# Performance work log

Measured on AMD Instinct MI355X. Metric: run time of the kernel, lower is better.

The kernel has to match this reference:

```python
import jax, jax.numpy as jnp
import numpy as np

B, NPG, A, E = 128, 512, 8, 504   # graphs, nodes/graph, agents, edges/graph
F_IN, HID, H = 3, 64, 8
C = HID
F = H * C                          # 512 = concat head output
OUT = 2
NEG_SLOPE = 0.2


def _seg_softmax(alpha, dst, n):
    # edge-softmax normalized over destination-node neighborhoods
    m = jax.ops.segment_max(alpha, dst, num_segments=n)
    e = jnp.exp(alpha - m[dst])
    s = jax.ops.segment_sum(e, dst, num_segments=n)
    return e / jnp.clip(s[dst], 1e-16)


def _gat(x, src, dst, ea, W, b, a_s, a_d, We, a_e, n, self_loops):
    # PyG GATConv: heads=H, concat=True, edge_dim=1, fill_value='mean'
    xs = (x @ W).reshape(n, H, C)                      # [N,H,C]
    als = jnp.einsum('nhc,hc->nh', xs, a_s)            # alpha_src per node
    ald = jnp.einsum('nhc,hc->nh', xs, a_d)            # alpha_dst per node
    if self_loops:
        # fill_value='mean': self-loop attr = mean of incoming edge attrs
        ssum = jax.ops.segment_sum(ea, dst, num_segments=n)
        cnt = jax.ops.segment_sum(jnp.ones((dst.shape[0], 1), ea.dtype), dst, num_segments=n)
        loop_attr = ssum / jnp.maximum(cnt, 1.0)
        ea = jnp.concatenate([ea, loop_attr], axis=0)
        loop = jnp.arange(n, dtype=src.dtype)
        src = jnp.concatenate([src, loop])
        dst = jnp.concatenate([dst, loop])
    ee = (ea @ We).reshape(-1, H, C)                   # lin_edge
    ale = jnp.einsum('ehc,hc->eh', ee, a_e)            # alpha_edge per edge
    alpha = jax.nn.leaky_relu(als[src] + ald[dst] + ale, NEG_SLOPE)  # [E,H]
    alpha = _seg_softmax(alpha, dst, n)
    out = jax.ops.segment_sum(alpha[:, :, None] * xs[src], dst, num_segments=n)
    return out.reshape(n, H * C) + b


def _forward(x, edge_index, edge_attr, p1, p2, p3, fc1_w, fc1_b, fc2_w, fc2_b):
    Bq, npg, _ = x.shape
    n = Bq * npg
    off = (jnp.arange(Bq, dtype=edge_index.dtype) * npg)[:, None]   # PyG Batch offsets
    src = (edge_index[..., 0] + off).reshape(-1)
    dst = (edge_index[..., 1] + off).reshape(-1)
    ea = edge_attr.reshape(-1, 1)
    h = x.reshape(n, -1)
    h = jax.nn.relu(_gat(h, src, dst, ea, *p1, n, False))   # conv1: add_self_loops=False
    h = jax.nn.relu(_gat(h, src, dst, ea, *p2, n, True))
    h = jax.nn.relu(_gat(h, src, dst, ea, *p3, n, True))
    hg = h.reshape(Bq, npg, F)
    graph_emb = hg.mean(axis=1)                      # global_mean_pool (equal-size graphs)
    agent_emb = hg[:, :A].reshape(Bq * A, F)         # first num_agents nodes per graph
    comb = jnp.concatenate([agent_emb, jnp.repeat(graph_emb, A, axis=0)], axis=1)
    comb = jax.nn.relu(comb @ fc1_w + fc1_b)         # fc1 ReLU (extra torch.relu is idempotent)
    pred = comb @ fc2_w + fc2_b
    return pred.reshape(Bq, A, OUT)


def setup_inputs() -> dict:
    key = jax.random.key(0)
    ks = jax.random.split(key, 32)
    rn = lambda i, shape: jax.random.normal(ks[i], shape, jnp.float32) * 0.05
    inp = {
        'x': jax.random.normal(ks[0], (B, NPG, F_IN), jnp.float32),
        'edge_index': jax.random.randint(ks[1], (B, E, 2), 0, NPG, jnp.int32),
        'edge_attr': jax.random.normal(ks[2], (B, E, 1), jnp.float32),
    }
    dims = [F_IN, F, F]
    for li, din in enumerate(dims, start=1):
        inp[f'W{li}'] = rn(3 + li * 6, (din, H * C))
        inp[f'b{li}'] = jnp.zeros((H * C,), jnp.float32)
        inp[f'as{li}'] = rn(4 + li * 6, (H, C))
        inp[f'ad{li}'] = rn(5 + li * 6, (H, C))
        inp[f'We{li}'] = rn(6 + li * 6, (1, H * C))
        inp[f'ae{li}'] = rn(7 + li * 6, (H, C))
    inp['fc1_w'] = rn(28, (2 * F, 4 * HID))
    inp['fc1_b'] = jnp.zeros((4 * HID,), jnp.float32)
    inp['fc2_w'] = rn(29, (4 * HID, OUT))
    inp['fc2_b'] = jnp.zeros((OUT,), jnp.float32)
    return inp


def reference(x, edge_index, edge_attr,
              W1, b1, as1, ad1, We1, ae1,
              W2, b2, as2, ad2, We2, ae2,
              W3, b3, as3, ad3, We3, ae3,
              fc1_w, fc1_b, fc2_w, fc2_b):
    p1 = (W1, b1, as1, ad1, We1, ae1)
    p2 = (W2, b2, as2, ad2, We2, ae2)
    p3 = (W3, b3, as3, ad3, We3, ae3)
    return _forward(x, edge_index, edge_attr, p1, p2, p3, fc1_w, fc1_b, fc2_w, fc2_b)
```

## Files before the change

kernel.cpp:

```cpp
#include <hip/hip_runtime.h>
#include <hip/hip_bf16.h>
#include <math.h>

#define NGRAPH 128
#define NPG_   512
#define NN     (NGRAPH*NPG_)
#define EPG    504
#define ETOT   (NGRAPH*EPG)
#define HEADS  8
#define FDIM   512
#define NEG    0.2f

typedef __hip_bfloat16 bf16;
typedef __attribute__((ext_vector_type(8))) short short8;
typedef __attribute__((ext_vector_type(4))) float f32x4;

static __device__ __forceinline__ float bf(short s){
  union { unsigned u; float f; } c; c.u = ((unsigned)(unsigned short)s) << 16; return c.f;
}
static __device__ __forceinline__ short fbf(float v){
  bf16 b = __float2bfloat16(v); return *(short*)&b;
}

static __device__ __forceinline__ void gload16(void* lds, const void* g){
  __builtin_amdgcn_global_load_lds((const __attribute__((address_space(1))) void*)g,
                                   (__attribute__((address_space(3))) void*)lds, 16, 0, 0);
}

__global__ void k_sentinel(float* out, int n){
  int i = blockIdx.x*blockDim.x + threadIdx.x;
  if (i < n) out[i] = 12345.0f;
}

__global__ __launch_bounds__(512) void k_csr(const int* __restrict__ ei, const float* __restrict__ ea,
                                             const float* __restrict__ We0, const float* __restrict__ ae0,
                                             const float* __restrict__ We1, const float* __restrict__ ae1,
                                             const float* __restrict__ We2, const float* __restrict__ ae2,
                                             int* __restrict__ deg_g, int* __restrict__ row_ptr,
                                             float* __restrict__ la,
                                             int* __restrict__ esrc, float* __restrict__ eattr,
                                             float* __restrict__ coef){
  int b = blockIdx.x;
  int t = threadIdx.x;
  if (b >= NGRAPH){
    int l = b - NGRAPH;
    const float* We = l==0 ? We0 : (l==1 ? We1 : We2);
    const float* ae = l==0 ? ae0 : (l==1 ? ae1 : ae2);
    float v = We[t]*ae[t];
    #pragma unroll
    for (int o=32;o>0;o>>=1) v += __shfl_down(v, o);
    if ((t & 63) == 0) coef[l*HEADS + (t>>6)] = v;
    return;
  }
  __shared__ int   dg[512];
  __shared__ float ss[512];
  __shared__ int   scan[512];
  __shared__ int   cur[512];
  dg[t] = 0; ss[t] = 0.f;
  __syncthreads();
  int src=0, dst=0; float at=0.f;
  if (t < EPG){
    src = ei[(b*EPG+t)*2];
    dst = ei[(b*EPG+t)*2+1];
    at  = ea[b*EPG+t];
    atomicAdd(&dg[dst], 1);
    atomicAdd(&ss[dst], at);
  }
  __syncthreads();
  int d = dg[t];
  scan[t] = d;
  __syncthreads();
  for (int o=1;o<512;o<<=1){
    int v2 = (t>=o) ? scan[t-o] : 0;
    __syncthreads();
    scan[t] += v2;
    __syncthreads();
  }
  int excl = scan[t] - d;
  int n = b*NPG_ + t;
  row_ptr[n] = b*EPG + excl;
  deg_g[n]   = d;
  la[n]      = ss[t] / fmaxf((float)d, 1.f);
  cur[t] = excl;
  __syncthreads();
  if (t < EPG){
    int slot = atomicAdd(&cur[dst], 1);
    int p = b*EPG + slot;
    esrc[p]  = b*NPG_ + src;
    eattr[p] = at;
  }
}

__global__ void k_wt(const float* __restrict__ W1, const float* __restrict__ W2,
                     bf16* __restrict__ wt){
  int idx = blockIdx.x*blockDim.x + threadIdx.x;
  if (idx >= 2*FDIM*FDIM) return;
  int l = idx >> 18;
  int r = idx & (FDIM*FDIM-1);
  int n = r >> 9, k = r & 511;
  const float* W = l ? W2 : W1;
  wt[idx] = __float2bfloat16(W[k*FDIM + n]);
}

__global__ __launch_bounds__(256) void k_gat1(const float* __restrict__ x,
                                              const float* __restrict__ W,
                                              const float* __restrict__ a_s,
                                              const float* __restrict__ a_d,
                                              const float* __restrict__ coef,
                                              const int* __restrict__ row_ptr,
                                              const int* __restrict__ deg,
                                              const int* __restrict__ esrc,
                                              const float* __restrict__ eattr,
                                              const float* __restrict__ bias,
                                              bf16* __restrict__ h){
  int nwg = gridDim.x;
  int cpx = nwg >> 3;
  int bid = blockIdx.x;
  int swz = (bid & 7)*cpx + (bid >> 3);
  int n = swz*4 + (threadIdx.x >> 6);
  int lane = threadIdx.x & 63;
  int hh = lane >> 3;
  int f0 = lane << 3;

  float w0[8], w1[8], w2[8], as8[8], ad8[8];
  #pragma unroll
  for (int j=0;j<8;j+=4){
    *(float4*)&w0[j]  = *(const float4*)&W[f0+j];
    *(float4*)&w1[j]  = *(const float4*)&W[FDIM+f0+j];
    *(float4*)&w2[j]  = *(const float4*)&W[2*FDIM+f0+j];
    *(float4*)&as8[j] = *(const float4*)&a_s[f0+j];
    *(float4*)&ad8[j] = *(const float4*)&a_d[f0+j];
  }

  const float* xr = x + n*3;
  float x0 = xr[0], x1 = xr[1], x2 = xr[2];
  float dsum = 0.f;
  #pragma unroll
  for (int j=0;j<8;j++){
    float v = x0*w0[j] + x1*w1[j] + x2*w2[j];
    dsum += v*ad8[j];
  }
  #pragma unroll
  for (int o=1;o<8;o<<=1) dsum += __shfl_xor(dsum, o);
  float aldn = dsum;
  float ch = coef[hh];

  int row = row_ptr[n], d = deg[n];
  float m = -1e30f, ssum = 0.f;
  float acc[8] = {};
  for (int i=0;i<d;i++){
    int s = esrc[row+i]; float at = eattr[row+i];
    const float* xsr = x + s*3;
    float y0 = xsr[0], y1 = xsr[1], y2 = xsr[2];
    float v[8]; float ssrc = 0.f;
    #pragma unroll
    for (int j=0;j<8;j++){
      v[j] = y0*w0[j] + y1*w1[j] + y2*w2[j];
      ssrc += v[j]*as8[j];
    }
    #pragma unroll
    for (int o=1;o<8;o<<=1) ssrc += __shfl_xor(ssrc, o);
    float raw = ssrc + aldn + at*ch;
    raw = raw > 0.f ? raw : NEG*raw;
    float mn = fmaxf(m, raw);
    float sc = __expf(m - mn);
    float p  = __expf(raw - mn);
    ssum = ssum*sc + p;
    #pragma unroll
    for (int j=0;j<8;j++) acc[j] = acc[j]*sc + p*v[j];
    m = mn;
  }
  float inv = 1.f / fmaxf(ssum, 1e-16f);
  short8 r;
  #pragma unroll
  for (int j=0;j<8;j++){
    float o = acc[j]*inv + bias[f0+j];
    r[j] = fbf(o > 0.f ? o : 0.f);
  }
  ((short8*)(h + (size_t)n*FDIM))[lane] = r;
}

__global__ __launch_bounds__(256) void k_attn_node(const bf16* __restrict__ xs,
                                                   const float* __restrict__ a_s,
                                                   const float* __restrict__ a_d,
                                                   float* __restrict__ als,
                                                   float* __restrict__ ald){
  int n = blockIdx.x*4 + (threadIdx.x >> 6);
  int lane = threadIdx.x & 63;
  short8 v = ((const short8*)(xs + (size_t)n*FDIM))[lane];
  const float4* as4 = (const float4*)a_s;
  const float4* ad4 = (const float4*)a_d;
  float4 sa = as4[lane*2], sb = as4[lane*2+1];
  float4 da = ad4[lane*2], db = ad4[lane*2+1];
  float s = bf(v[0])*sa.x + bf(v[1])*sa.y + bf(v[2])*sa.z + bf(v[3])*sa.w
          + bf(v[4])*sb.x + bf(v[5])*sb.y + bf(v[6])*sb.z + bf(v[7])*sb.w;
  float d = bf(v[0])*da.x + bf(v[1])*da.y + bf(v[2])*da.z + bf(v[3])*da.w
          + bf(v[4])*db.x + bf(v[5])*db.y + bf(v[6])*db.z + bf(v[7])*db.w;
  #pragma unroll
  for (int o=1;o<8;o<<=1){ s += __shfl_xor(s, o); d += __shfl_xor(d, o); }
  if ((lane & 7) == 0){
    int hh = lane >> 3;
    als[n*HEADS+hh] = s;
    ald[n*HEADS+hh] = d;
  }
}

__global__ __launch_bounds__(256) void k_gat(const bf16* __restrict__ xs,
                                             const float* __restrict__ als,
                                             const float* __restrict__ ald,
                                             const float* __restrict__ coef,
                                             const int* __restrict__ row_ptr,
                                             const int* __restrict__ deg,
                                             const int* __restrict__ esrc,
                                             const float* __restrict__ eattr,
                                             const float* __restrict__ la,
                                             const float* __restrict__ bias,
                                             bf16* __restrict__ h){
  int nwg = gridDim.x;
  int cpx = nwg >> 3;
  int bid = blockIdx.x;
  int swz = (bid & 7)*cpx + (bid >> 3);
  int n = swz*4 + (threadIdx.x >> 6);
  int lane = threadIdx.x & 63;
  int hh = lane >> 3;
  int row = row_ptr[n], d = deg[n];
  int tot = d + 1;
  float aldn = ald[n*HEADS+hh];
  float ch = coef[hh];
  float lan = la[n];

  float m = -1e30f, ssum = 0.f;
  float acc[8] = {};
  for (int i=0;i<tot;i++){
    int s; float at;
    if (i<d){ s = esrc[row+i]; at = eattr[row+i]; }
    else    { s = n;           at = lan; }
    float raw = als[s*HEADS+hh] + aldn + at*ch;
    raw = raw > 0.f ? raw : NEG*raw;
    float mn = fmaxf(m, raw);
    float scale = __expf(m - mn);
    float p = __expf(raw - mn);
    ssum = ssum*scale + p;
    short8 v = ((const short8*)(xs + (size_t)s*FDIM))[lane];
    #pragma unroll
    for (int j=0;j<8;j++) acc[j] = acc[j]*scale + p*bf(v[j]);
    m = mn;
  }
  float inv = 1.f / fmaxf(ssum, 1e-16f);
  const float4* b4 = (const float4*)bias;
  float4 ba = b4[lane*2], bb = b4[lane*2+1];
  float bias8[8] = {ba.x,ba.y,ba.z,ba.w,bb.x,bb.y,bb.z,bb.w};
  short8 r;
  #pragma unroll
  for (int j=0;j<8;j++){
    float o = acc[j]*inv + bias8[j];
    r[j] = fbf(o > 0.f ? o : 0.f);
  }
  ((short8*)(h + (size_t)n*FDIM))[lane] = r;
}

__global__ __launch_bounds__(256) void gemm_mfma(const bf16* __restrict__ A,
                                                 const bf16* __restrict__ Wt,
                                                 bf16* __restrict__ C,
                                                 int M, int N, int K){
  __shared__ short As[128*64];
  __shared__ short Bs[128*64];
  int bid = blockIdx.x;
  int wk = ((bid & 7) << 8) | (bid >> 3);
  const int bm = (wk >> 2)*128, bn = (wk & 3)*128;
  const int tid = threadIdx.x;
  const int lane = tid & 63;
  const int w = tid >> 6;
  const int wm = (w >> 1)*64, wn = (w & 1)*64;
  const int lr = lane & 15;
  const int lk = lane >> 4;

  f32x4 acc[4][4] = {};

  for (int k0 = 0; k0 < K; k0 += 64){
    #pragma unroll
    for (int is = 0; is < 4; ++is){
      int i = is*256 + tid;
      int r = i >> 3, g = i & 7;
      int gs = g ^ (r & 7);
      gload16(&As[i*8], A  + (size_t)(bm+r)*K + k0 + gs*8);
      gload16(&Bs[i*8], Wt + (size_t)(bn+r)*K + k0 + gs*8);
    }
    __syncthreads();
    #pragma unroll
    for (int kk = 0; kk < 2; ++kk){
      short8 af[4], bfr[4];
      #pragma unroll
      for (int mi=0; mi<4; ++mi){
        int row = wm + mi*16 + lr;
        int g = (kk*4 + lk) ^ (row & 7);
        af[mi] = *(const short8*)&As[row*64 + g*8];
      }
      #pragma unroll
      for (int ni=0; ni<4; ++ni){
        int row = wn + ni*16 + lr;
        int g = (kk*4 + lk) ^ (row & 7);
        bfr[ni] = *(const short8*)&Bs[row*64 + g*8];
      }
      #pragma unroll
      for (int mi=0; mi<4; ++mi)
        #pragma unroll
        for (int ni=0; ni<4; ++ni)
          acc[mi][ni] = __builtin_amdgcn_mfma_f32_16x16x32_bf16(af[mi], bfr[ni], acc[mi][ni], 0,0,0);
    }
    __syncthreads();
  }

  #pragma unroll
  for (int mi=0; mi<4; ++mi)
    #pragma unroll
    for (int ni=0; ni<4; ++ni){
      int col = bn + wn + ni*16 + lr;
      #pragma unroll
      for (int r=0; r<4; ++r){
        int rowg = bm + wm + mi*16 + lk*4 + r;
        C[(size_t)rowg*N + col] = __float2bfloat16(acc[mi][ni][r]);
      }
    }
}

__global__ __launch_bounds__(256) void k_gemb1(const bf16* __restrict__ h, float* __restrict__ pgemb){
  int gs_ = blockIdx.x;
  int g = gs_ >> 3, s = gs_ & 7;
  int t = threadIdx.x;
  int c = t & 63, rg = t >> 6;
  const bf16* base = h + ((size_t)(g*NPG_ + s*64 + rg*16))*FDIM;
  float acc[8] = {};
  #pragma unroll 4
  for (int i=0;i<16;i++){
    short8 v = ((const short8*)(base + (size_t)i*FDIM))[c];
    #pragma unroll
    for (int j=0;j<8;j++) acc[j] += bf(v[j]);
  }
  float* dst = pgemb + ((size_t)(gs_*4 + rg))*FDIM + c*8;
  float4 lo = {acc[0],acc[1],acc[2],acc[3]};
  float4 hi = {acc[4],acc[5],acc[6],acc[7]};
  *(float4*)dst = lo;
  *(float4*)(dst+4) = hi;
}

__global__ __launch_bounds__(1024) void k_head(const bf16* __restrict__ h,
                                               const float* __restrict__ pgemb,
                                               const float* __restrict__ fc1w,
                                               const float* __restrict__ fc1b,
                                               const float* __restrict__ fc2w,
                                               const float* __restrict__ fc2b,
                                               float* __restrict__ out){
  __shared__ float ge[FDIM];
  __shared__ float ag[8][FDIM];
  __shared__ float ps[2][8][257];
  __shared__ float gs2[2][256];
  __shared__ float f1[8][256];
  int g = blockIdx.x, t = threadIdx.x;

  if (t < FDIM){
    float s = 0.f;
    const float* p = pgemb + (size_t)g*32*FDIM + t;
    #pragma unroll
    for (int c=0;c<32;c++) s += p[(size_t)c*FDIM];
    ge[t] = s * (1.f/NPG_);
  } else {
    int i = t - FDIM;
    int r = i >> 6, c = i & 63;
    short8 v = ((const short8*)(h + (size_t)(g*NPG_ + r)*FDIM))[c];
    #pragma unroll
    for (int j=0;j<8;j++) ag[r][c*8+j] = bf(v[j]);
  }
  __syncthreads();

  int col = t & 255, q = t >> 8;
  if (q < 2){
    float acc[8] = {};
    int kbeg = q*256;
    for (int k = kbeg; k < kbeg+256; k += 4){
      float w0 = fc1w[(k+0)*256+col];
      float w1 = fc1w[(k+1)*256+col];
      float w2 = fc1w[(k+2)*256+col];
      float w3 = fc1w[(k+3)*256+col];
      #pragma unroll
      for (int r=0;r<8;r++){
        float4 a = *(const float4*)&ag[r][k];
        acc[r] += a.x*w0 + a.y*w1 + a.z*w2 + a.w*w3;
      }
    }
    #pragma unroll
    for (int r=0;r<8;r++) ps[q][r][col] = acc[r];
  } else {
    float gacc = 0.f;
    int kbeg = (q-2)*256;
    for (int k = kbeg; k < kbeg+256; k += 4){
      float v0 = fc1w[(FDIM+k+0)*256+col];
      float v1 = fc1w[(FDIM+k+1)*256+col];
      float v2 = fc1w[(FDIM+k+2)*256+col];
      float v3 = fc1w[(FDIM+k+3)*256+col];
      float4 gv = *(const float4*)&ge[k];
      gacc += gv.x*v0 + gv.y*v1 + gv.z*v2 + gv.w*v3;
    }
    gs2[q-2][col] = gacc;
  }
  __syncthreads();

  if (t < 256){
    float b = fc1b[t] + gs2[0][t] + gs2[1][t];
    #pragma unroll
    for (int r=0;r<8;r++)
      f1[r][t] = fmaxf(ps[0][r][t] + ps[1][r][t] + b, 0.f);
  }
  __syncthreads();

  if (t < 128){
    int r = t >> 4, o = (t >> 3) & 1, l = t & 7;
    float s = 0.f;
    for (int k = l; k < 256; k += 8) s += f1[r][k] * fc2w[k*2+o];
    #pragma unroll
    for (int off=4; off; off>>=1) s += __shfl_down(s, off);
    if (l == 0) out[(g*8 + r)*2 + o] = s + fc2b[o];
  }
}

extern "C" void kernel_launch(void* const* d_in, const int* in_sizes, int n_in,
                              void* d_out, int out_size, void* d_ws, size_t ws_size,
                              hipStream_t stream)
{
  const float* x    = (const float*)d_in[0];
  const int*   ei   = (const int*)  d_in[1];
  const float* ea   = (const float*)d_in[2];
  const float* Wl[3]  = {(const float*)d_in[3],  (const float*)d_in[9],  (const float*)d_in[15]};
  const float* Bl[3]  = {(const float*)d_in[4],  (const float*)d_in[10], (const float*)d_in[16]};
  const float* ASl[3] = {(const float*)d_in[5],  (const float*)d_in[11], (const float*)d_in[17]};
  const float* ADl[3] = {(const float*)d_in[6],  (const float*)d_in[12], (const float*)d_in[18]};
  const float* WEl[3] = {(const float*)d_in[7],  (const float*)d_in[13], (const float*)d_in[19]};
  const float* AEl[3] = {(const float*)d_in[8],  (const float*)d_in[14], (const float*)d_in[20]};
  const float* FC1W = (const float*)d_in[21];
  const float* FC1B = (const float*)d_in[22];
  const float* FC2W = (const float*)d_in[23];
  const float* FC2B = (const float*)d_in[24];
  float* out = (float*)d_out;
  (void)in_sizes; (void)n_in;

  char* ws = (char*)d_ws;
  size_t off = 0;
  auto alloc = [&](size_t bytes)->char*{
    char* p = ws + off;
    off = (off + bytes + 255) & ~(size_t)255;
    return p;
  };
  bf16*  h       = (bf16*) alloc((size_t)NN*FDIM*2);
  bf16*  xs      = (bf16*) alloc((size_t)NN*FDIM*2);
  float* als     = (float*)alloc((size_t)NN*HEADS*4);
  float* ald     = (float*)alloc((size_t)NN*HEADS*4);
  float* la      = (float*)alloc((size_t)NN*4);
  int*   deg     = (int*)  alloc((size_t)NN*4);
  int*   row_ptr = (int*)  alloc((size_t)NN*4);
  int*   esrc    = (int*)  alloc((size_t)ETOT*4);
  float* eattr   = (float*)alloc((size_t)ETOT*4);
  float* coef    = (float*)alloc(3*HEADS*4);
  bf16*  wt      = (bf16*) alloc((size_t)2*FDIM*FDIM*2);
  float* pgemb   = (float*)alloc((size_t)NGRAPH*32*FDIM*4);

  if (off > ws_size){
    k_sentinel<<<(out_size+255)/256, 256, 0, stream>>>(out, out_size);
    return;
  }

  k_csr<<<NGRAPH+3, 512, 0, stream>>>(ei, ea, WEl[0], AEl[0], WEl[1], AEl[1], WEl[2], AEl[2],
                                      deg, row_ptr, la, esrc, eattr, coef);
  k_wt<<<(2*FDIM*FDIM+255)/256, 256, 0, stream>>>(Wl[1], Wl[2], wt);

  k_gat1<<<NN/4, 256, 0, stream>>>(x, Wl[0], ASl[0], ADl[0], coef, row_ptr, deg, esrc, eattr, Bl[0], h);

  for (int l=1;l<3;l++){
    gemm_mfma<<<2048, 256, 0, stream>>>(h, wt + (size_t)(l-1)*FDIM*FDIM, xs, NN, FDIM, FDIM);
    k_attn_node<<<NN/4, 256, 0, stream>>>(xs, ASl[l], ADl[l], als, ald);
    k_gat<<<NN/4, 256, 0, stream>>>(xs, als, ald, coef + l*HEADS, row_ptr, deg, esrc, eattr, la, Bl[l], h);
  }

  k_gemb1<<<NGRAPH*8, 256, 0, stream>>>(h, pgemb);
  k_head <<<NGRAPH, 1024, 0, stream>>>(h, pgemb, FC1W, FC1B, FC2W, FC2B, out);
}
```

Baseline: 265.5 us.

## Aggregate raw 3-dim inputs before projection in first GAT layer

```diff
diff --git a/kernel.cpp b/kernel.cpp
--- a/kernel.cpp
+++ b/kernel.cpp
@@ -36,20 +36,38 @@
                                              const float* __restrict__ We0, const float* __restrict__ ae0,
                                              const float* __restrict__ We1, const float* __restrict__ ae1,
                                              const float* __restrict__ We2, const float* __restrict__ ae2,
+                                             const float* __restrict__ W1,
+                                             const float* __restrict__ as1, const float* __restrict__ ad1,
                                              int* __restrict__ deg_g, int* __restrict__ row_ptr,
                                              float* __restrict__ la,
                                              int* __restrict__ esrc, float* __restrict__ eattr,
-                                             float* __restrict__ coef){
+                                             float* __restrict__ coef, float* __restrict__ wsd){
   int b = blockIdx.x;
   int t = threadIdx.x;
   if (b >= NGRAPH){
-    int l = b - NGRAPH;
-    const float* We = l==0 ? We0 : (l==1 ? We1 : We2);
-    const float* ae = l==0 ? ae0 : (l==1 ? ae1 : ae2);
-    float v = We[t]*ae[t];
-    #pragma unroll
-    for (int o=32;o>0;o>>=1) v += __shfl_down(v, o);
-    if ((t & 63) == 0) coef[l*HEADS + (t>>6)] = v;
+    if (b < NGRAPH+3){
+      int l = b - NGRAPH;
+      const float* We = l==0 ? We0 : (l==1 ? We1 : We2);
+      const float* ae = l==0 ? ae0 : (l==1 ? ae1 : ae2);
+      float v = We[t]*ae[t];
+      #pragma unroll
+      for (int o=32;o>0;o>>=1) v += __shfl_down(v, o);
+      if ((t & 63) == 0) coef[l*HEADS + (t>>6)] = v;
+      return;
+    }
+    float as_v = as1[t], ad_v = ad1[t];
+    float v[6] = { W1[t]*as_v, W1[512+t]*as_v, W1[1024+t]*as_v,
+                   W1[t]*ad_v, W1[512+t]*ad_v, W1[1024+t]*ad_v };
+    #pragma unroll
+    for (int o=32;o>0;o>>=1){
+      #pragma unroll
+      for (int q=0;q<6;q++) v[q] += __shfl_down(v[q], o);
+    }
+    if ((t & 63) == 0){
+      int w = t >> 6;
+      wsd[w*3+0]    = v[0]; wsd[w*3+1]    = v[1]; wsd[w*3+2]    = v[2];
+      wsd[24+w*3+0] = v[3]; wsd[24+w*3+1] = v[4]; wsd[24+w*3+2] = v[5];
+    }
     return;
   }
   __shared__ int   dg[512];
@@ -104,8 +122,7 @@
 
 __global__ __launch_bounds__(256) void k_gat1(const float* __restrict__ x,
                                               const float* __restrict__ W,
-                                              const float* __restrict__ a_s,
-                                              const float* __restrict__ a_d,
+                                              const float* __restrict__ wsd,
                                               const float* __restrict__ coef,
                                               const int* __restrict__ row_ptr,
                                               const int* __restrict__ deg,
@@ -122,59 +139,46 @@
   int hh = lane >> 3;
   int f0 = lane << 3;
 
-  float w0[8], w1[8], w2[8], as8[8], ad8[8];
-  #pragma unroll
-  for (int j=0;j<8;j+=4){
-    *(float4*)&w0[j]  = *(const float4*)&W[f0+j];
-    *(float4*)&w1[j]  = *(const float4*)&W[FDIM+f0+j];
-    *(float4*)&w2[j]  = *(const float4*)&W[2*FDIM+f0+j];
-    *(float4*)&as8[j] = *(const float4*)&a_s[f0+j];
-    *(float4*)&ad8[j] = *(const float4*)&a_d[f0+j];
-  }
+  float ws0 = wsd[hh*3+0],    ws1 = wsd[hh*3+1],    ws2 = wsd[hh*3+2];
+  float wd0 = wsd[24+hh*3+0], wd1 = wsd[24+hh*3+1], wd2 = wsd[24+hh*3+2];
+  float ch = coef[hh];
 
   const float* xr = x + n*3;
-  float x0 = xr[0], x1 = xr[1], x2 = xr[2];
-  float dsum = 0.f;
-  #pragma unroll
-  for (int j=0;j<8;j++){
-    float v = x0*w0[j] + x1*w1[j] + x2*w2[j];
-    dsum += v*ad8[j];
-  }
-  #pragma unroll
-  for (int o=1;o<8;o<<=1) dsum += __shfl_xor(dsum, o);
-  float aldn = dsum;
-  float ch = coef[hh];
+  float aldn = xr[0]*wd0 + xr[1]*wd1 + xr[2]*wd2;
 
   int row = row_ptr[n], d = deg[n];
   float m = -1e30f, ssum = 0.f;
-  float acc[8] = {};
+  float a0 = 0.f, a1 = 0.f, a2 = 0.f;
   for (int i=0;i<d;i++){
     int s = esrc[row+i]; float at = eattr[row+i];
     const float* xsr = x + s*3;
     float y0 = xsr[0], y1 = xsr[1], y2 = xsr[2];
-    float v[8]; float ssrc = 0.f;
-    #pragma unroll
-    for (int j=0;j<8;j++){
-      v[j] = y0*w0[j] + y1*w1[j] + y2*w2[j];
-      ssrc += v[j]*as8[j];
-    }
-    #pragma unroll
-    for (int o=1;o<8;o<<=1) ssrc += __shfl_xor(ssrc, o);
-    float raw = ssrc + aldn + at*ch;
+    float raw = y0*ws0 + y1*ws1 + y2*ws2 + aldn + at*ch;
     raw = raw > 0.f ? raw : NEG*raw;
     float mn = fmaxf(m, raw);
     float sc = __expf(m - mn);
     float p  = __expf(raw - mn);
     ssum = ssum*sc + p;
-    #pragma unroll
-    for (int j=0;j<8;j++) acc[j] = acc[j]*sc + p*v[j];
+    a0 = a0*sc + p*y0;
+    a1 = a1*sc + p*y1;
+    a2 = a2*sc + p*y2;
     m = mn;
   }
   float inv = 1.f / fmaxf(ssum, 1e-16f);
+  a0 *= inv; a1 *= inv; a2 *= inv;
+
+  float w0[8], w1[8], w2[8], b8[8];
+  #pragma unroll
+  for (int j=0;j<8;j+=4){
+    *(float4*)&w0[j] = *(const float4*)&W[f0+j];
+    *(float4*)&w1[j] = *(const float4*)&W[FDIM+f0+j];
+    *(float4*)&w2[j] = *(const float4*)&W[2*FDIM+f0+j];
+    *(float4*)&b8[j] = *(const float4*)&bias[f0+j];
+  }
   short8 r;
   #pragma unroll
   for (int j=0;j<8;j++){
-    float o = acc[j]*inv + bias[f0+j];
+    float o = a0*w0[j] + a1*w1[j] + a2*w2[j] + b8[j];
     r[j] = fbf(o > 0.f ? o : 0.f);
   }
   ((short8*)(h + (size_t)n*FDIM))[lane] = r;
@@ -460,6 +464,7 @@
   int*   esrc    = (int*)  alloc((size_t)ETOT*4);
   float* eattr   = (float*)alloc((size_t)ETOT*4);
   float* coef    = (float*)alloc(3*HEADS*4);
+  float* wsd     = (float*)alloc(48*4);
   bf16*  wt      = (bf16*) alloc((size_t)2*FDIM*FDIM*2);
   float* pgemb   = (float*)alloc((size_t)NGRAPH*32*FDIM*4);
 
@@ -468,11 +473,12 @@
     return;
   }
 
-  k_csr<<<NGRAPH+3, 512, 0, stream>>>(ei, ea, WEl[0], AEl[0], WEl[1], AEl[1], WEl[2], AEl[2],
-                                      deg, row_ptr, la, esrc, eattr, coef);
+  k_csr<<<NGRAPH+4, 512, 0, stream>>>(ei, ea, WEl[0], AEl[0], WEl[1], AEl[1], WEl[2], AEl[2],
+                                      Wl[0], ASl[0], ADl[0],
+                                      deg, row_ptr, la, esrc, eattr, coef, wsd);
   k_wt<<<(2*FDIM*FDIM+255)/256, 256, 0, stream>>>(Wl[1], Wl[2], wt);
 
-  k_gat1<<<NN/4, 256, 0, stream>>>(x, Wl[0], ASl[0], ADl[0], coef, row_ptr, deg, esrc, eattr, Bl[0], h);
+  k_gat1<<<NN/4, 256, 0, stream>>>(x, Wl[0], wsd, coef, row_ptr, deg, esrc, eattr, Bl[0], h);
 
   for (int l=1;l<3;l++){
     gemm_mfma<<<2048, 256, 0, stream>>>(h, wt + (size_t)(l-1)*FDIM*FDIM, xs, NN, FDIM, FDIM);
```

Measured after the change: 255.1 us. 1.04x faster.
